# Optimization experiments

Measured on AMD Instinct MI355X. Metric: run time of the kernel, lower is better.

The kernel has to match this reference:

```python
import jax, jax.numpy as jnp
import numpy as np

N, V, H = 2048, 204, 160
LN_EPS = 1e-5


def setup_inputs() -> dict:
    key = jax.random.key(0)
    ks = jax.random.split(key, 5)
    x = jax.random.normal(ks[0], (N, V, 1), dtype=jnp.float32)
    fc1_w = jax.random.normal(ks[1], (V, H), dtype=jnp.float32) * 0.02
    fc1_b = jnp.zeros((V, H), dtype=jnp.float32)
    fc2_w = jax.random.normal(ks[2], (V, H, H), dtype=jnp.float32) * 0.02
    fc2_b = jnp.zeros((V, H), dtype=jnp.float32)
    glu_w = jax.random.normal(ks[3], (V, 2 * H, H), dtype=jnp.float32) * 0.02
    glu_b = jnp.zeros((V, 2 * H), dtype=jnp.float32)
    skip_w = jax.random.normal(ks[4], (V, H), dtype=jnp.float32) * 0.02
    skip_b = jnp.zeros((V, H), dtype=jnp.float32)
    ln_gamma = jnp.ones((H,), dtype=jnp.float32)
    ln_beta = jnp.zeros((H,), dtype=jnp.float32)
    return {"x": x, "fc1_w": fc1_w, "fc1_b": fc1_b, "fc2_w": fc2_w,
            "fc2_b": fc2_b, "glu_w": glu_w, "glu_b": glu_b,
            "skip_w": skip_w, "skip_b": skip_b,
            "ln_gamma": ln_gamma, "ln_beta": ln_beta}


def reference(x, fc1_w, fc1_b, fc2_w, fc2_b, glu_w, glu_b, skip_w, skip_b,
              ln_gamma, ln_beta):
    # x: (N, V, 1) -> xs: (N, V)
    xs = x[..., 0]
    # broadcast linear (var_dim=1 -> H): (N, V, H)
    h = jax.nn.elu(xs[:, :, None] * fc1_w[None] + fc1_b[None])
    # per-variable H x H GEMM: bmm over V
    h = jnp.einsum('nvh,vhk->nvk', h, fc2_w) + fc2_b[None]
    # GLU projection: (N, V, 2H)  (matches bmm(h, glu_w.transpose(1,2)))
    glu = jnp.einsum('nvh,vgh->nvg', h, glu_w) + glu_b[None]
    fc_out, gate = glu[..., :H], glu[..., H:]
    h = fc_out * jax.nn.sigmoid(gate)  # dropout is identity at eval
    # skip path (broadcast linear)
    skip = xs[:, :, None] * skip_w[None] + skip_b[None]
    y = skip + h
    # LayerNorm over last dim
    mu = jnp.mean(y, axis=-1, keepdims=True)
    var = jnp.mean(jnp.square(y - mu), axis=-1, keepdims=True)
    yhat = (y - mu) * jax.lax.rsqrt(var + LN_EPS)
    return yhat * ln_gamma + ln_beta
```

## Files before the change

### kernel.cpp

```cpp
#include <hip/hip_runtime.h>

#define N_TOK 2048
#define V_DIM 204
#define H_DIM 160
#define G_DIM 320
#define BM 64
#define LN_EPSF 1e-5f

typedef short s8v __attribute__((ext_vector_type(8)));
typedef unsigned short u16x8 __attribute__((ext_vector_type(8)));
typedef float f32x4 __attribute__((ext_vector_type(4)));

#define IMG_SUB 51200
#define IMG_PER_V (3 * IMG_SUB)

typedef unsigned int __attribute__((address_space(1))) as1_u32;
typedef unsigned int __attribute__((address_space(3))) as3_u32;

__device__ __forceinline__ void gl_lds16(const void* g, void* l) {
    __builtin_amdgcn_global_load_lds((as1_u32*)g, (as3_u32*)l, 16, 0, 0);
}

__device__ __forceinline__ unsigned short f2bf(float f) {
    union { float f; unsigned int u; } a;
    a.f = f;
    unsigned int r = a.u + 0x7fffu + ((a.u >> 16) & 1u);
    return (unsigned short)(r >> 16);
}

__global__ __launch_bounds__(256) void prep_weights(const float* __restrict__ fc2_w,
                                                    const float* __restrict__ glu_w,
                                                    unsigned short* __restrict__ ws) {
    int b = blockIdx.x;
    int v = b >> 2, p = b & 3;
    int t = threadIdx.x;
    char* img = (char*)ws + (size_t)v * IMG_PER_V;
    if (p < 2) {
        __shared__ float tile[H_DIM][81];
        const float* w1 = fc2_w + (size_t)v * H_DIM * H_DIM + p * 80;
        for (int i = t; i < H_DIM * 80; i += 256) {
            int r = i / 80, c = i % 80;
            tile[r][c] = w1[(size_t)r * H_DIM + c];
        }
        __syncthreads();
        for (int c2 = t; c2 < 20 * 80; c2 += 256) {
            int chunk = c2 / 80, ko = c2 % 80;
            u16x8 pk;
            #pragma unroll
            for (int j = 0; j < 8; j++) pk[j] = f2bf(tile[chunk * 8 + j][ko]);
            *(u16x8*)(img + (size_t)(chunk * 160 + p * 80 + ko) * 16) = pk;
        }
    } else {
        int half = p - 2;
        const float* w2 = glu_w + (size_t)v * G_DIM * H_DIM + (size_t)half * H_DIM * H_DIM;
        char* dst = img + IMG_SUB + (size_t)half * IMG_SUB;
        for (int c = t; c < 3200; c += 256) {
            int grow = c / 20, chunk = c % 20;
            const float* src = w2 + (size_t)grow * H_DIM + chunk * 8;
            f32x4 lo = *(const f32x4*)src;
            f32x4 hi = *(const f32x4*)(src + 4);
            u16x8 pk;
            #pragma unroll
            for (int j = 0; j < 4; j++) { pk[j] = f2bf(lo[j]); pk[4 + j] = f2bf(hi[j]); }
            *(u16x8*)(dst + (size_t)(chunk * 160 + grow) * 16) = pk;
        }
    }
}

__global__ __launch_bounds__(256, 2) void grn_main(
    const float* __restrict__ x,
    const float* __restrict__ fc1_w, const float* __restrict__ fc1_b,
    const float* __restrict__ fc2_b, const float* __restrict__ glu_b,
    const float* __restrict__ skip_w, const float* __restrict__ skip_b,
    const float* __restrict__ ln_g, const float* __restrict__ ln_b,
    const unsigned short* __restrict__ ws, float* __restrict__ out)
{
    __shared__ __align__(16) unsigned short w_lds[20 * 160 * 8];
    __shared__ __align__(16) unsigned short hc_lds[20 * 64 * 8];

    int bid = blockIdx.x;
    int swb = (bid & 7) * 816 + (bid >> 3);
    int v  = swb >> 5;
    int n0 = (swb & 31) * BM;

    int t = threadIdx.x;
    int lane = t & 63;
    int wv = t >> 6;
    int wr = wv >> 1;
    int wc = wv & 1;
    int col = lane & 15;
    int kg  = lane >> 4;

    const char* img = (const char*)ws + (size_t)v * IMG_PER_V;

    for (int i = t; i < 3200; i += 256)
        gl_lds16(img + (size_t)i * 16, (char*)w_lds + i * 16);

    const float* fw = fc1_w + v * H_DIM;
    const float* fb = fc1_b + v * H_DIM;
    for (int i = t; i < 20 * BM; i += 256) {
        int chunk = i >> 6, row = i & 63;
        float xv = x[(size_t)(n0 + row) * V_DIM + v];
        int k0 = chunk * 8;
        u16x8 pk;
        #pragma unroll
        for (int j = 0; j < 8; j++) {
            float z = xv * fw[k0 + j] + fb[k0 + j];
            float e = z > 0.f ? z : (__expf(z) - 1.f);
            pk[j] = f2bf(e);
        }
        *(u16x8*)((char*)hc_lds + chunk * 1024 + row * 16) = pk;
    }
    __syncthreads();

    int arow = wr * 32 + col;

    s8v a1[2][5];
    #pragma unroll
    for (int m = 0; m < 2; m++)
        #pragma unroll
        for (int kk = 0; kk < 5; kk++)
            a1[m][kk] = *(const s8v*)((const char*)hc_lds +
                         (kk * 4 + kg) * 1024 + (arow + m * 16) * 16);

    f32x4 acc[2][5];
    #pragma unroll
    for (int m = 0; m < 2; m++)
        #pragma unroll
        for (int n = 0; n < 5; n++) acc[m][n] = (f32x4){0.f, 0.f, 0.f, 0.f};

    #pragma unroll
    for (int kk = 0; kk < 5; kk++) {
        s8v b[5];
        #pragma unroll
        for (int n = 0; n < 5; n++)
            b[n] = *(const s8v*)((const char*)w_lds +
                    (kk * 4 + kg) * 2560 + (wc * 80 + n * 16 + col) * 16);
        #pragma unroll
        for (int n = 0; n < 5; n++)
            #pragma unroll
            for (int m = 0; m < 2; m++)
                acc[m][n] = __builtin_amdgcn_mfma_f32_16x16x32_bf16(a1[m][kk], b[n], acc[m][n], 0, 0, 0);
    }
    __syncthreads();

    for (int i = t; i < 3200; i += 256)
        gl_lds16(img + IMG_SUB + (size_t)i * 16, (char*)w_lds + i * 16);

    const float* f2b = fc2_b + v * H_DIM;
    #pragma unroll
    for (int n = 0; n < 5; n++) {
        int gc = wc * 80 + n * 16 + col;
        float bias = f2b[gc];
        int cbase = (gc >> 3) * 1024 + (gc & 7) * 2;
        #pragma unroll
        for (int m = 0; m < 2; m++)
            #pragma unroll
            for (int j = 0; j < 4; j++) {
                int row = wr * 32 + m * 16 + kg * 4 + j;
                *(unsigned short*)((char*)hc_lds + cbase + row * 16) = f2bf(acc[m][n][j] + bias);
            }
    }
    __syncthreads();

    s8v a2[2][5];
    #pragma unroll
    for (int m = 0; m < 2; m++)
        #pragma unroll
        for (int kk = 0; kk < 5; kk++)
            a2[m][kk] = *(const s8v*)((const char*)hc_lds +
                         (kk * 4 + kg) * 1024 + (arow + m * 16) * 16);

    f32x4 af[2][5];
    #pragma unroll
    for (int m = 0; m < 2; m++)
        #pragma unroll
        for (int n = 0; n < 5; n++) af[m][n] = (f32x4){0.f, 0.f, 0.f, 0.f};

    #pragma unroll
    for (int kk = 0; kk < 5; kk++) {
        s8v b[5];
        #pragma unroll
        for (int n = 0; n < 5; n++)
            b[n] = *(const s8v*)((const char*)w_lds +
                    (kk * 4 + kg) * 2560 + (wc * 80 + n * 16 + col) * 16);
        #pragma unroll
        for (int n = 0; n < 5; n++)
            #pragma unroll
            for (int m = 0; m < 2; m++)
                af[m][n] = __builtin_amdgcn_mfma_f32_16x16x32_bf16(a2[m][kk], b[n], af[m][n], 0, 0, 0);
    }
    __syncthreads();

    for (int i = t; i < 3200; i += 256)
        gl_lds16(img + 2 * IMG_SUB + (size_t)i * 16, (char*)w_lds + i * 16);

    const float* gb  = glu_b + v * G_DIM;
    const float* sw_ = skip_w + v * H_DIM;
    const float* sb_ = skip_b + v * H_DIM;
    float bfo[5], bga[5], sww[5], sbb[5], lng[5], lnb[5];
    #pragma unroll
    for (int n = 0; n < 5; n++) {
        int gc = wc * 80 + n * 16 + col;
        bfo[n] = gb[gc]; bga[n] = gb[H_DIM + gc];
        sww[n] = sw_[gc]; sbb[n] = sb_[gc];
        lng[n] = ln_g[gc]; lnb[n] = ln_b[gc];
    }
    float xrow[2][4];
    #pragma unroll
    for (int m = 0; m < 2; m++)
        #pragma unroll
        for (int j = 0; j < 4; j++)
            xrow[m][j] = x[(size_t)(n0 + wr * 32 + m * 16 + kg * 4 + j) * V_DIM + v];
    __syncthreads();

    f32x4 ag[2][5];
    #pragma unroll
    for (int m = 0; m < 2; m++)
        #pragma unroll
        for (int n = 0; n < 5; n++) ag[m][n] = (f32x4){0.f, 0.f, 0.f, 0.f};

    #pragma unroll
    for (int kk = 0; kk < 5; kk++) {
        s8v b[5];
        #pragma unroll
        for (int n = 0; n < 5; n++)
            b[n] = *(const s8v*)((const char*)w_lds +
                    (kk * 4 + kg) * 2560 + (wc * 80 + n * 16 + col) * 16);
        #pragma unroll
        for (int n = 0; n < 5; n++)
            #pragma unroll
            for (int m = 0; m < 2; m++)
                ag[m][n] = __builtin_amdgcn_mfma_f32_16x16x32_bf16(a2[m][kk], b[n], ag[m][n], 0, 0, 0);
    }

    float y[2][5][4];
    float sum[2][4] = {}, ssq[2][4] = {};
    #pragma unroll
    for (int n = 0; n < 5; n++) {
        #pragma unroll
        for (int m = 0; m < 2; m++)
            #pragma unroll
            for (int j = 0; j < 4; j++) {
                float fo = af[m][n][j] + bfo[n];
                float ga = ag[m][n][j] + bga[n];
                float hh = fo / (1.f + __expf(-ga));
                float yv = xrow[m][j] * sww[n] + sbb[n] + hh;
                y[m][n][j] = yv;
                sum[m][j] += yv;
                ssq[m][j] += yv * yv;
            }
    }
    #pragma unroll
    for (int msk = 1; msk < 16; msk <<= 1)
        #pragma unroll
        for (int m = 0; m < 2; m++)
            #pragma unroll
            for (int j = 0; j < 4; j++) {
                sum[m][j] += __shfl_xor(sum[m][j], msk, 64);
                ssq[m][j] += __shfl_xor(ssq[m][j], msk, 64);
            }

    float2* red = (float2*)hc_lds;
    if (col == 0) {
        #pragma unroll
        for (int m = 0; m < 2; m++)
            #pragma unroll
            for (int j = 0; j < 4; j++) {
                int row = wr * 32 + m * 16 + kg * 4 + j;
                red[row * 2 + wc] = make_float2(sum[m][j], ssq[m][j]);
            }
    }
    __syncthreads();

    float mu_[2][4], rs_[2][4];
    #pragma unroll
    for (int m = 0; m < 2; m++)
        #pragma unroll
        for (int j = 0; j < 4; j++) {
            int row = wr * 32 + m * 16 + kg * 4 + j;
            f32x4 p = *(const f32x4*)&red[row * 2];
            float mu = (p[0] + p[2]) * (1.f / H_DIM);
            float var = (p[1] + p[3]) * (1.f / H_DIM) - mu * mu;
            mu_[m][j] = mu;
            rs_[m][j] = rsqrtf(var + LN_EPSF);
        }

    #pragma unroll
    for (int n = 0; n < 5; n++) {
        int gc = wc * 80 + n * 16 + col;
        #pragma unroll
        for (int m = 0; m < 2; m++)
            #pragma unroll
            for (int j = 0; j < 4; j++) {
                int row = n0 + wr * 32 + m * 16 + kg * 4 + j;
                out[((size_t)row * V_DIM + v) * H_DIM + gc] =
                    (y[m][n][j] - mu_[m][j]) * rs_[m][j] * lng[n] + lnb[n];
            }
    }
}

__global__ __launch_bounds__(160) void grn_fallback(
    const float* __restrict__ x,
    const float* __restrict__ fc1_w, const float* __restrict__ fc1_b,
    const float* __restrict__ fc2_w, const float* __restrict__ fc2_b,
    const float* __restrict__ glu_w, const float* __restrict__ glu_b,
    const float* __restrict__ skip_w, const float* __restrict__ skip_b,
    const float* __restrict__ ln_g, const float* __restrict__ ln_b,
    float* __restrict__ out)
{
    int n = blockIdx.x / V_DIM, v = blockIdx.x % V_DIM;
    int k = threadIdx.x;
    __shared__ float hb[H_DIM], c1[H_DIM], yb[H_DIM];
    float xv = x[(size_t)n * V_DIM + v];
    float z = xv * fc1_w[v * H_DIM + k] + fc1_b[v * H_DIM + k];
    hb[k] = z > 0.f ? z : (__expf(z) - 1.f);
    __syncthreads();
    const float* w1 = fc2_w + (size_t)v * H_DIM * H_DIM;
    float s = fc2_b[v * H_DIM + k];
    for (int i = 0; i < H_DIM; i++) s += hb[i] * w1[(size_t)i * H_DIM + k];
    c1[k] = s;
    __syncthreads();
    const float* w2 = glu_w + (size_t)v * G_DIM * H_DIM;
    float sf = glu_b[v * G_DIM + k], sg = glu_b[v * G_DIM + H_DIM + k];
    for (int i = 0; i < H_DIM; i++) {
        float cv = c1[i];
        sf += cv * w2[(size_t)k * H_DIM + i];
        sg += cv * w2[(size_t)(k + H_DIM) * H_DIM + i];
    }
    float y = xv * skip_w[v * H_DIM + k] + skip_b[v * H_DIM + k] + sf / (1.f + __expf(-sg));
    yb[k] = y;
    __syncthreads();
    float sum = 0.f, ssq = 0.f;
    for (int i = 0; i < H_DIM; i++) { sum += yb[i]; ssq += yb[i] * yb[i]; }
    float mu = sum / H_DIM;
    float var = ssq / H_DIM - mu * mu;
    out[((size_t)n * V_DIM + v) * H_DIM + k] =
        (y - mu) * rsqrtf(var + LN_EPSF) * ln_g[k] + ln_b[k];
}

extern "C" void kernel_launch(void* const* d_in, const int* in_sizes, int n_in,
                              void* d_out, int out_size, void* d_ws, size_t ws_size,
                              hipStream_t stream) {
    const float* x      = (const float*)d_in[0];
    const float* fc1_w  = (const float*)d_in[1];
    const float* fc1_b  = (const float*)d_in[2];
    const float* fc2_w  = (const float*)d_in[3];
    const float* fc2_b  = (const float*)d_in[4];
    const float* glu_w  = (const float*)d_in[5];
    const float* glu_b  = (const float*)d_in[6];
    const float* skip_w = (const float*)d_in[7];
    const float* skip_b = (const float*)d_in[8];
    const float* ln_g   = (const float*)d_in[9];
    const float* ln_b   = (const float*)d_in[10];
    float* out = (float*)d_out;

    size_t need = (size_t)V_DIM * IMG_PER_V;
    if (ws_size >= need) {
        unsigned short* ws = (unsigned short*)d_ws;
        prep_weights<<<V_DIM * 4, 256, 0, stream>>>(fc2_w, glu_w, ws);
        grn_main<<<V_DIM * (N_TOK / BM), 256, 0, stream>>>(
            x, fc1_w, fc1_b, fc2_b, glu_b, skip_w, skip_b, ln_g, ln_b, ws, out);
    } else {
        grn_fallback<<<N_TOK * V_DIM, 160, 0, stream>>>(
            x, fc1_w, fc1_b, fc2_w, fc2_b, glu_w, glu_b, skip_w, skip_b, ln_g, ln_b, out);
    }
}
```

Baseline: 541.9 us.

## Read weight B-fragments directly from global memory instead of staging through LDS

```diff
diff --git a/kernel.cpp b/kernel.cpp
--- a/kernel.cpp
+++ b/kernel.cpp
@@ -14,18 +14,17 @@
 #define IMG_SUB 51200
 #define IMG_PER_V (3 * IMG_SUB)
 
-typedef unsigned int __attribute__((address_space(1))) as1_u32;
-typedef unsigned int __attribute__((address_space(3))) as3_u32;
-
-__device__ __forceinline__ void gl_lds16(const void* g, void* l) {
-    __builtin_amdgcn_global_load_lds((as1_u32*)g, (as3_u32*)l, 16, 0, 0);
-}
-
 __device__ __forceinline__ unsigned short f2bf(float f) {
     union { float f; unsigned int u; } a;
     a.f = f;
     unsigned int r = a.u + 0x7fffu + ((a.u >> 16) & 1u);
     return (unsigned short)(r >> 16);
+}
+
+__device__ __forceinline__ unsigned short f2bf_fast(float f) {
+    union { float f; unsigned int u; } a;
+    a.f = f;
+    return (unsigned short)((a.u + 0x8000u) >> 16);
 }
 
 __global__ __launch_bounds__(256) void prep_weights(const float* __restrict__ fc2_w,
@@ -67,7 +66,7 @@
     }
 }
 
-__global__ __launch_bounds__(256, 2) void grn_main(
+__global__ __launch_bounds__(256, 3) void grn_main(
     const float* __restrict__ x,
     const float* __restrict__ fc1_w, const float* __restrict__ fc1_b,
     const float* __restrict__ fc2_b, const float* __restrict__ glu_b,
@@ -75,8 +74,8 @@
     const float* __restrict__ ln_g, const float* __restrict__ ln_b,
     const unsigned short* __restrict__ ws, float* __restrict__ out)
 {
-    __shared__ __align__(16) unsigned short w_lds[20 * 160 * 8];
     __shared__ __align__(16) unsigned short hc_lds[20 * 64 * 8];
+    __shared__ __align__(16) float2 red_lds[BM * 2];
 
     int bid = blockIdx.x;
     int swb = (bid & 7) * 816 + (bid >> 3);
@@ -92,9 +91,7 @@
     int kg  = lane >> 4;
 
     const char* img = (const char*)ws + (size_t)v * IMG_PER_V;
-
-    for (int i = t; i < 3200; i += 256)
-        gl_lds16(img + (size_t)i * 16, (char*)w_lds + i * 16);
+    const char* bbase = img + kg * 2560 + (wc * 80 + col) * 16;
 
     const float* fw = fc1_w + v * H_DIM;
     const float* fb = fc1_b + v * H_DIM;
@@ -107,7 +104,7 @@
         for (int j = 0; j < 8; j++) {
             float z = xv * fw[k0 + j] + fb[k0 + j];
             float e = z > 0.f ? z : (__expf(z) - 1.f);
-            pk[j] = f2bf(e);
+            pk[j] = f2bf_fast(e);
         }
         *(u16x8*)((char*)hc_lds + chunk * 1024 + row * 16) = pk;
     }
@@ -134,8 +131,7 @@
         s8v b[5];
         #pragma unroll
         for (int n = 0; n < 5; n++)
-            b[n] = *(const s8v*)((const char*)w_lds +
-                    (kk * 4 + kg) * 2560 + (wc * 80 + n * 16 + col) * 16);
+            b[n] = *(const s8v*)(bbase + kk * 10240 + n * 256);
         #pragma unroll
         for (int n = 0; n < 5; n++)
             #pragma unroll
@@ -143,9 +139,6 @@
                 acc[m][n] = __builtin_amdgcn_mfma_f32_16x16x32_bf16(a1[m][kk], b[n], acc[m][n], 0, 0, 0);
     }
     __syncthreads();
-
-    for (int i = t; i < 3200; i += 256)
-        gl_lds16(img + IMG_SUB + (size_t)i * 16, (char*)w_lds + i * 16);
 
     const float* f2b = fc2_b + v * H_DIM;
     #pragma unroll
@@ -158,7 +151,7 @@
             #pragma unroll
             for (int j = 0; j < 4; j++) {
                 int row = wr * 32 + m * 16 + kg * 4 + j;
-                *(unsigned short*)((char*)hc_lds + cbase + row * 16) = f2bf(acc[m][n][j] + bias);
+                *(unsigned short*)((char*)hc_lds + cbase + row * 16) = f2bf_fast(acc[m][n][j] + bias);
             }
     }
     __syncthreads();
@@ -182,18 +175,32 @@
         s8v b[5];
         #pragma unroll
         for (int n = 0; n < 5; n++)
-            b[n] = *(const s8v*)((const char*)w_lds +
-                    (kk * 4 + kg) * 2560 + (wc * 80 + n * 16 + col) * 16);
+            b[n] = *(const s8v*)(bbase + IMG_SUB + kk * 10240 + n * 256);
         #pragma unroll
         for (int n = 0; n < 5; n++)
             #pragma unroll
             for (int m = 0; m < 2; m++)
                 af[m][n] = __builtin_amdgcn_mfma_f32_16x16x32_bf16(a2[m][kk], b[n], af[m][n], 0, 0, 0);
     }
-    __syncthreads();
-
-    for (int i = t; i < 3200; i += 256)
-        gl_lds16(img + 2 * IMG_SUB + (size_t)i * 16, (char*)w_lds + i * 16);
+
+    f32x4 ag[2][5];
+    #pragma unroll
+    for (int m = 0; m < 2; m++)
+        #pragma unroll
+        for (int n = 0; n < 5; n++) ag[m][n] = (f32x4){0.f, 0.f, 0.f, 0.f};
+
+    #pragma unroll
+    for (int kk = 0; kk < 5; kk++) {
+        s8v b[5];
+        #pragma unroll
+        for (int n = 0; n < 5; n++)
+            b[n] = *(const s8v*)(bbase + 2 * IMG_SUB + kk * 10240 + n * 256);
+        #pragma unroll
+        for (int n = 0; n < 5; n++)
+            #pragma unroll
+            for (int m = 0; m < 2; m++)
+                ag[m][n] = __builtin_amdgcn_mfma_f32_16x16x32_bf16(a2[m][kk], b[n], ag[m][n], 0, 0, 0);
+    }
 
     const float* gb  = glu_b + v * G_DIM;
     const float* sw_ = skip_w + v * H_DIM;
@@ -212,27 +219,6 @@
         #pragma unroll
         for (int j = 0; j < 4; j++)
             xrow[m][j] = x[(size_t)(n0 + wr * 32 + m * 16 + kg * 4 + j) * V_DIM + v];
-    __syncthreads();
-
-    f32x4 ag[2][5];
-    #pragma unroll
-    for (int m = 0; m < 2; m++)
-        #pragma unroll
-        for (int n = 0; n < 5; n++) ag[m][n] = (f32x4){0.f, 0.f, 0.f, 0.f};
-
-    #pragma unroll
-    for (int kk = 0; kk < 5; kk++) {
-        s8v b[5];
-        #pragma unroll
-        for (int n = 0; n < 5; n++)
-            b[n] = *(const s8v*)((const char*)w_lds +
-                    (kk * 4 + kg) * 2560 + (wc * 80 + n * 16 + col) * 16);
-        #pragma unroll
-        for (int n = 0; n < 5; n++)
-            #pragma unroll
-            for (int m = 0; m < 2; m++)
-                ag[m][n] = __builtin_amdgcn_mfma_f32_16x16x32_bf16(a2[m][kk], b[n], ag[m][n], 0, 0, 0);
-    }
 
     float y[2][5][4];
     float sum[2][4] = {}, ssq[2][4] = {};
@@ -261,14 +247,13 @@
                 ssq[m][j] += __shfl_xor(ssq[m][j], msk, 64);
             }
 
-    float2* red = (float2*)hc_lds;
     if (col == 0) {
         #pragma unroll
         for (int m = 0; m < 2; m++)
             #pragma unroll
             for (int j = 0; j < 4; j++) {
                 int row = wr * 32 + m * 16 + kg * 4 + j;
-                red[row * 2 + wc] = make_float2(sum[m][j], ssq[m][j]);
+                red_lds[row * 2 + wc] = make_float2(sum[m][j], ssq[m][j]);
             }
     }
     __syncthreads();
@@ -279,7 +264,7 @@
         #pragma unroll
         for (int j = 0; j < 4; j++) {
             int row = wr * 32 + m * 16 + kg * 4 + j;
-            f32x4 p = *(const f32x4*)&red[row * 2];
+            f32x4 p = *(const f32x4*)&red_lds[row * 2];
             float mu = (p[0] + p[2]) * (1.f / H_DIM);
             float var = (p[1] + p[3]) * (1.f / H_DIM) - mu * mu;
             mu_[m][j] = mu;
```

Measured after the change: 541.5 us. Within noise of the previous version (-0.1%).
